# Kernel tuning notes

Measured on AMD Instinct MI355X. Metric: run time of the kernel, lower is better.

## Reference

```python
import jax, jax.numpy as jnp
import numpy as np

B, T, V, K = 4, 1024, 32000, 50000
EPS_T, EPS_M = 1e-8, 1e-12


def setup_inputs() -> dict:
    key = jax.random.key(0)
    k1, k2, k3, k4 = jax.random.split(key, 4)
    probs = jax.random.uniform(k1, (B, T, V), dtype=jnp.float32)
    # normalize so rows are valid distributions (faithful to softmax outputs)
    probs = probs / probs.sum(-1, keepdims=True)
    target_probs = jax.random.uniform(k2, (K,), dtype=jnp.float32) * (1.0 / K)
    target_oov = jax.random.uniform(k3, (1,), dtype=jnp.float32)
    mask = jnp.ones((B, T), dtype=bool)
    pairs = jax.random.randint(k4, (K, 2), 0, V, dtype=jnp.int64 if jax.config.jax_enable_x64 else jnp.int32)
    return {"probs": probs, "target_probs": target_probs, "target_oov": target_oov,
            "mask": mask, "pairs": pairs}


def reference(probs, target_probs, target_oov, mask, pairs):
    a = pairs[:, 0]  # (K,)
    b = pairs[:, 1]
    p_t = probs[:, :-1, :]   # (B, T-1, V)
    p_t1 = probs[:, 1:, :]
    pair_mask = (mask[:, :-1] & mask[:, 1:]).astype(jnp.float32)  # (B, T-1)
    # gather bigram probs: (B, T-1, K) joint, masked sum over batch/seq
    joint = p_t[..., a] * p_t1[..., b]
    topk_sum = jnp.einsum('btk,bt->k', joint, pair_mask)  # (K,)
    n_pairs = pair_mask.sum()

    # finalize
    n = jnp.maximum(n_pairs, 1.0)
    model_top = jnp.maximum(topk_sum / n, EPS_M)
    model_oov = jnp.clip(1.0 - model_top.sum(), EPS_M, 1.0 - EPS_T)
    tgt = jnp.maximum(target_probs, EPS_T)
    t_oov = jnp.maximum(target_oov[0], EPS_T)
    kl_top = (model_top * (jnp.log(model_top) - jnp.log(tgt))).sum()
    kl_oov = model_oov * (jnp.log(model_oov) - jnp.log(t_oov))
    return kl_top + kl_oov
```

## Files before the change

### kernel.cpp

```cpp
#include <hip/hip_runtime.h>
#include <stdint.h>

#define B_   4
#define T_   1024
#define V_   32000
#define K_   50000
#define N_   (B_*(T_-1))
#define TPB  1024
#define U_   49
#define KP   (TPB*U_)
#define POS_PER_BLK 16
#define G1   ((N_ + POS_PER_BLK - 1)/POS_PER_BLK)
#define EPSTGT 1e-8f
#define EPSMOD 1e-12f
#define MAXSLOTS 64
#define W4   (V_/4)

__device__ __forceinline__ uint32_t bf16rne(float x) {
    uint32_t u = __float_as_uint(x);
    u += 0x7FFFu + ((u >> 16) & 1u);
    return u >> 16;
}
__device__ __forceinline__ uint2 pack4(float4 v) {
    uint2 pk;
    pk.x = bf16rne(v.x) | (bf16rne(v.y) << 16);
    pk.y = bf16rne(v.z) | (bf16rne(v.w) << 16);
    return pk;
}

__device__ __forceinline__ void stage_row(const float* __restrict__ probs, int r,
                                          ushort* dst, int tid) {
    const float4* src = (const float4*)(probs + (size_t)r * V_);
    for (int i = tid; i < W4; i += TPB) {
        *(uint2*)(dst + i * 4) = pack4(src[i]);
    }
}

__global__ void k_pack(const int* __restrict__ pairs, uint32_t* __restrict__ ppk) {
    int k = blockIdx.x * 256 + threadIdx.x;
    if (k >= KP) return;
    uint32_t v = 0;
    if (k < K_) {
        uint32_t a = (uint32_t)pairs[2 * k];
        uint32_t b = (uint32_t)pairs[2 * k + 1];
        v = ((a * 2u) << 16) | (b * 2u);
    }
    ppk[k] = v;
}

__global__ void k_mask(const unsigned char* __restrict__ mask, float* __restrict__ scalars) {
    __shared__ int red[16];
    int tid = threadIdx.x;
    int cnt = 0;
    for (int n = tid; n < N_; n += 1024) {
        int b = n / (T_ - 1);
        int t = n - b * (T_ - 1);
        int r = b * T_ + t;
        cnt += (mask[r] && mask[r + 1]) ? 1 : 0;
    }
    for (int off = 32; off > 0; off >>= 1) cnt += __shfl_down(cnt, off, 64);
    int wid = tid >> 6, lid = tid & 63;
    if (lid == 0) red[wid] = cnt;
    __syncthreads();
    if (tid == 0) {
        int s = 0;
        for (int w = 0; w < 16; ++w) s += red[w];
        scalars[0] = (float)s;
    }
}

__global__ __launch_bounds__(TPB) void k_main(
    const float* __restrict__ probs,
    const unsigned char* __restrict__ mask,
    const uint32_t* __restrict__ ppk,
    float* __restrict__ partials, int S)
{
    __shared__ __align__(16) ushort rows[2][V_];
    const int tid = threadIdx.x;
    const int g = blockIdx.x;
    const int n0 = g * POS_PER_BLK;
    const int n1 = min(N_, n0 + POS_PER_BLK);

    float acc[U_];
#pragma unroll
    for (int u = 0; u < U_; ++u) acc[u] = 0.f;

    int r0 = n0 + n0 / (T_ - 1);
    int r1 = r0 + 1;
    stage_row(probs, r0, rows[r0 & 1], tid);
    stage_row(probs, r1, rows[r1 & 1], tid);

    for (int n = n0; n < n1; ++n) {
        const int nn = n + 1;
        const bool more = (nn < n1);
        const int nr0 = nn + nn / (T_ - 1);
        const int nr1 = nr0 + 1;
        const int pre_row = more ? ((nr0 == r1) ? nr1 : nr0) : -1;
        const bool extra = more && (nr0 != r1);

        const float4* src = (const float4*)(probs + (size_t)((pre_row >= 0) ? pre_row : 0) * V_);
        float4 L0[4];
#pragma unroll
        for (int j = 0; j < 4; ++j) L0[j] = src[tid + j * TPB];

        __syncthreads();

        const bool active = mask[r0] && mask[r1];
        const ushort* rp = rows[r0 & 1];
        const ushort* rq = rows[r1 & 1];
        const uint32_t* pp = ppk + tid;

        if (active) {
#pragma unroll
            for (int c = 0; c < 28; c += 7) {
                uint32_t pk[7];
#pragma unroll
                for (int j = 0; j < 7; ++j) pk[j] = pp[(c + j) * TPB];
#pragma unroll
                for (int j = 0; j < 7; ++j) {
                    uint32_t ao = pk[j] >> 16;
                    uint32_t bo = pk[j] & 0xFFFFu;
                    ushort av = *(const ushort*)((const char*)rp + ao);
                    ushort bv = *(const ushort*)((const char*)rq + bo);
                    float af = __uint_as_float(((uint32_t)av) << 16);
                    float bf = __uint_as_float(((uint32_t)bv) << 16);
                    acc[c + j] = fmaf(af, bf, acc[c + j]);
                }
            }
        }

        uint2 P0[4];
#pragma unroll
        for (int j = 0; j < 4; ++j) P0[j] = pack4(L0[j]);
        float4 L1[4];
#pragma unroll
        for (int j = 0; j < 4; ++j) {
            int i = tid + (4 + j) * TPB;
            int ic = (i < W4) ? i : 0;
            L1[j] = src[ic];
        }

        if (active) {
#pragma unroll
            for (int c = 28; c < U_; c += 7) {
                uint32_t pk[7];
#pragma unroll
                for (int j = 0; j < 7; ++j) pk[j] = pp[(c + j) * TPB];
#pragma unroll
                for (int j = 0; j < 7; ++j) {
                    uint32_t ao = pk[j] >> 16;
                    uint32_t bo = pk[j] & 0xFFFFu;
                    ushort av = *(const ushort*)((const char*)rp + ao);
                    ushort bv = *(const ushort*)((const char*)rq + bo);
                    float af = __uint_as_float(((uint32_t)av) << 16);
                    float bf = __uint_as_float(((uint32_t)bv) << 16);
                    acc[c + j] = fmaf(af, bf, acc[c + j]);
                }
            }
        }

        __syncthreads();

        if (pre_row >= 0) {
            ushort* dst = rows[pre_row & 1];
#pragma unroll
            for (int j = 0; j < 4; ++j) {
                int i = tid + j * TPB;
                *(uint2*)(dst + i * 4) = P0[j];
            }
#pragma unroll
            for (int j = 0; j < 4; ++j) {
                int i = tid + (4 + j) * TPB;
                if (i < W4) *(uint2*)(dst + i * 4) = pack4(L1[j]);
            }
            if (extra) stage_row(probs, nr1, rows[nr1 & 1], tid);
        }

        r0 = nr0; r1 = nr1;
    }

    float* slot = partials + (size_t)(g % S) * KP;
#pragma unroll
    for (int u = 0; u < U_; ++u)
        atomicAdd(slot + u * TPB + tid, acc[u]);
}

__global__ void k_reduce(const float* __restrict__ partials, const float* __restrict__ tgt,
                         float* __restrict__ scalars, int S) {
    int k = blockIdx.x * 256 + threadIdx.x;
    float n = fmaxf(scalars[0], 1.0f);
    float mt = 0.f, term = 0.f;
    if (k < K_) {
        float ts = 0.f;
        for (int s = 0; s < S; ++s) ts += partials[(size_t)s * KP + k];
        mt = fmaxf(ts / n, EPSMOD);
        float tg = fmaxf(tgt[k], EPSTGT);
        term = mt * (__logf(mt) - __logf(tg));
    }
    for (int off = 32; off > 0; off >>= 1) {
        mt += __shfl_down(mt, off, 64);
        term += __shfl_down(term, off, 64);
    }
    __shared__ float rm[4], rt[4];
    int wid = threadIdx.x >> 6, lid = threadIdx.x & 63;
    if (lid == 0) { rm[wid] = mt; rt[wid] = term; }
    __syncthreads();
    if (threadIdx.x == 0) {
        float sm = 0.f, st = 0.f;
        for (int w = 0; w < 4; ++w) { sm += rm[w]; st += rt[w]; }
        atomicAdd(&scalars[1], sm);
        atomicAdd(&scalars[2], st);
    }
}

__global__ void k_final(const float* __restrict__ scalars, const float* __restrict__ toov,
                        float* __restrict__ out) {
    float S1 = scalars[1], S2 = scalars[2];
    float moov = 1.f - S1;
    moov = fminf(fmaxf(moov, EPSMOD), 1.f - EPSTGT);
    float tv = fmaxf(toov[0], EPSTGT);
    out[0] = S2 + moov * (__logf(moov) - __logf(tv));
}

extern "C" void kernel_launch(void* const* d_in, const int* in_sizes, int n_in,
                              void* d_out, int out_size, void* d_ws, size_t ws_size,
                              hipStream_t stream) {
    const float* probs = (const float*)d_in[0];
    const float* tgt   = (const float*)d_in[1];
    const float* toov  = (const float*)d_in[2];
    const unsigned char* mask = (const unsigned char*)d_in[3];
    const int* pairs   = (const int*)d_in[4];
    float* out = (float*)d_out;

    char* ws = (char*)d_ws;
    uint32_t* ppk = (uint32_t*)ws;
    size_t off_sc = (size_t)KP * 4;
    float* scalars = (float*)(ws + off_sc);
    size_t off_pt = off_sc + 256;
    float* partials = (float*)(ws + off_pt);

    long avail = (long)ws_size - (long)off_pt;
    int S = (int)(avail / ((long)KP * 4));
    if (S > MAXSLOTS) S = MAXSLOTS;
    if (S < 1) S = 1;

    hipMemsetAsync(ws + off_sc, 0, 256 + (size_t)S * KP * 4, stream);
    k_pack<<<(KP + 255) / 256, 256, 0, stream>>>(pairs, ppk);
    k_mask<<<1, 1024, 0, stream>>>(mask, scalars);
    k_main<<<G1, TPB, 0, stream>>>(probs, mask, ppk, partials, S);
    k_reduce<<<(K_ + 255) / 256, 256, 0, stream>>>(partials, tgt, scalars, S);
    k_final<<<1, 1, 0, stream>>>(scalars, toov, out);
}
```

Measured before the change: 747.7 us.

## Restructure k_main loads with sched barriers, shared mask, and direct partial stores

Loads the mask rows for the block into shared memory once, hoists the packed pair indices into larger register batches issued ahead of the row-prefetch loads, and pins the instruction order with sched_barrier. When the workspace is large enough for one slot per block, each block writes its partials with plain stores instead of atomics, which also drops the large memset. This trades higher register pressure and a longer k_reduce (G1 slots to sum) for fewer atomics and better latency hiding.

```diff
diff --git a/kernel.cpp b/kernel.cpp
--- a/kernel.cpp
+++ b/kernel.cpp
@@ -13,7 +13,6 @@
 #define G1   ((N_ + POS_PER_BLK - 1)/POS_PER_BLK)
 #define EPSTGT 1e-8f
 #define EPSMOD 1e-12f
-#define MAXSLOTS 64
 #define W4   (V_/4)
 
 __device__ __forceinline__ uint32_t bf16rne(float x) {
@@ -27,7 +26,6 @@
     pk.y = bf16rne(v.z) | (bf16rne(v.w) << 16);
     return pk;
 }
-
 __device__ __forceinline__ void stage_row(const float* __restrict__ probs, int r,
                                           ushort* dst, int tid) {
     const float4* src = (const float4*)(probs + (size_t)r * V_);
@@ -35,6 +33,14 @@
         *(uint2*)(dst + i * 4) = pack4(src[i]);
     }
 }
+
+#define GATHER(pkv, accv) do {                                          \
+    uint32_t ao_ = (pkv) >> 16, bo_ = (pkv) & 0xFFFFu;                  \
+    ushort av_ = *(const ushort*)(rp + ao_);                            \
+    ushort bv_ = *(const ushort*)(rq + bo_);                            \
+    accv = fmaf(__uint_as_float((uint32_t)av_ << 16),                   \
+                __uint_as_float((uint32_t)bv_ << 16), accv);            \
+} while (0)
 
 __global__ void k_pack(const int* __restrict__ pairs, uint32_t* __restrict__ ppk) {
     int k = blockIdx.x * 256 + threadIdx.x;
@@ -73,22 +79,32 @@
     const float* __restrict__ probs,
     const unsigned char* __restrict__ mask,
     const uint32_t* __restrict__ ppk,
-    float* __restrict__ partials, int S)
+    float* __restrict__ partials, int S, int direct)
 {
     __shared__ __align__(16) ushort rows[2][V_];
+    __shared__ unsigned char mask_s[32];
     const int tid = threadIdx.x;
     const int g = blockIdx.x;
     const int n0 = g * POS_PER_BLK;
     const int n1 = min(N_, n0 + POS_PER_BLK);
 
-    float acc[U_];
-#pragma unroll
-    for (int u = 0; u < U_; ++u) acc[u] = 0.f;
-
     int r0 = n0 + n0 / (T_ - 1);
     int r1 = r0 + 1;
+    const int rbase = r0;
+    {
+        int rlast = (n1 - 1) + (n1 - 1) / (T_ - 1) + 1;
+        int nrows = rlast - rbase + 1;
+        if (tid < nrows) mask_s[tid] = mask[rbase + tid];
+    }
+
+    float acc[U_];
+#pragma unroll
+    for (int u = 0; u < U_; ++u) acc[u] = 0.f;
+
     stage_row(probs, r0, rows[r0 & 1], tid);
     stage_row(probs, r1, rows[r1 & 1], tid);
+
+    const uint32_t* pp = ppk + tid;
 
     for (int n = n0; n < n1; ++n) {
         const int nn = n + 1;
@@ -97,38 +113,36 @@
         const int nr1 = nr0 + 1;
         const int pre_row = more ? ((nr0 == r1) ? nr1 : nr0) : -1;
         const bool extra = more && (nr0 != r1);
-
-        const float4* src = (const float4*)(probs + (size_t)((pre_row >= 0) ? pre_row : 0) * V_);
+        const int ld_row = (pre_row >= 0) ? pre_row : 0;
+        const float4* src = (const float4*)(probs + (size_t)ld_row * V_);
+
+        __syncthreads();
+
+        uint32_t pkA[28];
+#pragma unroll
+        for (int j = 0; j < 28; ++j) pkA[j] = pp[j * TPB];
+        __builtin_amdgcn_sched_barrier(0);
         float4 L0[4];
 #pragma unroll
         for (int j = 0; j < 4; ++j) L0[j] = src[tid + j * TPB];
-
-        __syncthreads();
-
-        const bool active = mask[r0] && mask[r1];
-        const ushort* rp = rows[r0 & 1];
-        const ushort* rq = rows[r1 & 1];
-        const uint32_t* pp = ppk + tid;
+        __builtin_amdgcn_sched_barrier(0);
+
+        const bool active = mask_s[r0 - rbase] && mask_s[r1 - rbase];
+        const char* rp = (const char*)rows[r0 & 1];
+        const char* rq = (const char*)rows[r1 & 1];
 
         if (active) {
 #pragma unroll
-            for (int c = 0; c < 28; c += 7) {
-                uint32_t pk[7];
-#pragma unroll
-                for (int j = 0; j < 7; ++j) pk[j] = pp[(c + j) * TPB];
-#pragma unroll
-                for (int j = 0; j < 7; ++j) {
-                    uint32_t ao = pk[j] >> 16;
-                    uint32_t bo = pk[j] & 0xFFFFu;
-                    ushort av = *(const ushort*)((const char*)rp + ao);
-                    ushort bv = *(const ushort*)((const char*)rq + bo);
-                    float af = __uint_as_float(((uint32_t)av) << 16);
-                    float bf = __uint_as_float(((uint32_t)bv) << 16);
-                    acc[c + j] = fmaf(af, bf, acc[c + j]);
-                }
-            }
-        }
-
+            for (int j = 0; j < 14; ++j) GATHER(pkA[j], acc[j]);
+        }
+        uint32_t pkB[21];
+#pragma unroll
+        for (int j = 0; j < 21; ++j) pkB[j] = pp[(28 + j) * TPB];
+        __builtin_amdgcn_sched_barrier(0);
+        if (active) {
+#pragma unroll
+            for (int j = 14; j < 28; ++j) GATHER(pkA[j], acc[j]);
+        }
         uint2 P0[4];
 #pragma unroll
         for (int j = 0; j < 4; ++j) P0[j] = pack4(L0[j]);
@@ -136,27 +150,12 @@
 #pragma unroll
         for (int j = 0; j < 4; ++j) {
             int i = tid + (4 + j) * TPB;
-            int ic = (i < W4) ? i : 0;
-            L1[j] = src[ic];
-        }
-
+            L1[j] = src[(i < W4) ? i : 0];
+        }
+        __builtin_amdgcn_sched_barrier(0);
         if (active) {
 #pragma unroll
-            for (int c = 28; c < U_; c += 7) {
-                uint32_t pk[7];
-#pragma unroll
-                for (int j = 0; j < 7; ++j) pk[j] = pp[(c + j) * TPB];
-#pragma unroll
-                for (int j = 0; j < 7; ++j) {
-                    uint32_t ao = pk[j] >> 16;
-                    uint32_t bo = pk[j] & 0xFFFFu;
-                    ushort av = *(const ushort*)((const char*)rp + ao);
-                    ushort bv = *(const ushort*)((const char*)rq + bo);
-                    float af = __uint_as_float(((uint32_t)av) << 16);
-                    float bf = __uint_as_float(((uint32_t)bv) << 16);
-                    acc[c + j] = fmaf(af, bf, acc[c + j]);
-                }
-            }
+            for (int j = 0; j < 21; ++j) GATHER(pkB[j], acc[28 + j]);
         }
 
         __syncthreads();
@@ -164,10 +163,8 @@
         if (pre_row >= 0) {
             ushort* dst = rows[pre_row & 1];
 #pragma unroll
-            for (int j = 0; j < 4; ++j) {
-                int i = tid + j * TPB;
-                *(uint2*)(dst + i * 4) = P0[j];
-            }
+            for (int j = 0; j < 4; ++j)
+                *(uint2*)(dst + (tid + j * TPB) * 4) = P0[j];
 #pragma unroll
             for (int j = 0; j < 4; ++j) {
                 int i = tid + (4 + j) * TPB;
@@ -175,14 +172,18 @@
             }
             if (extra) stage_row(probs, nr1, rows[nr1 & 1], tid);
         }
-
         r0 = nr0; r1 = nr1;
     }
 
-    float* slot = partials + (size_t)(g % S) * KP;
-#pragma unroll
-    for (int u = 0; u < U_; ++u)
-        atomicAdd(slot + u * TPB + tid, acc[u]);
+    if (direct) {
+        float* slot = partials + (size_t)g * KP;
+#pragma unroll
+        for (int u = 0; u < U_; ++u) slot[u * TPB + tid] = acc[u];
+    } else {
+        float* slot = partials + (size_t)(g % S) * KP;
+#pragma unroll
+        for (int u = 0; u < U_; ++u) atomicAdd(slot + u * TPB + tid, acc[u]);
+    }
 }
 
 __global__ void k_reduce(const float* __restrict__ partials, const float* __restrict__ tgt,
@@ -240,14 +241,15 @@
     float* partials = (float*)(ws + off_pt);
 
     long avail = (long)ws_size - (long)off_pt;
-    int S = (int)(avail / ((long)KP * 4));
-    if (S > MAXSLOTS) S = MAXSLOTS;
-    if (S < 1) S = 1;
-
-    hipMemsetAsync(ws + off_sc, 0, 256 + (size_t)S * KP * 4, stream);
+    int smax = (int)(avail / ((long)KP * 4));
+    int direct = (smax >= G1) ? 1 : 0;
+    int S = direct ? G1 : (smax < 1 ? 1 : (smax > 64 ? 64 : smax));
+
+    hipMemsetAsync(ws + off_sc, 0, 256, stream);
+    if (!direct) hipMemsetAsync(partials, 0, (size_t)S * KP * 4, stream);
     k_pack<<<(KP + 255) / 256, 256, 0, stream>>>(pairs, ppk);
     k_mask<<<1, 1024, 0, stream>>>(mask, scalars);
-    k_main<<<G1, TPB, 0, stream>>>(probs, mask, ppk, partials, S);
+    k_main<<<G1, TPB, 0, stream>>>(probs, mask, ppk, partials, S, direct);
     k_reduce<<<(K_ + 255) / 256, 256, 0, stream>>>(partials, tgt, scalars, S);
     k_final<<<1, 1, 0, stream>>>(scalars, toov, out);
 }
```

Result: no change. 735.4 us (-1.6%).
